# Kernel optimization log

Measured on AMD Instinct MI355X. Metric: run time of the kernel, lower is better.

## Reference

```python
import jax, jax.numpy as jnp
import numpy as np

N = 100000      # nodes
E = 1600000     # edges
F_IN = 256      # nfeat
F_OUT = 128     # out channels


def setup_inputs() -> dict:
    key = jax.random.key(0)
    k1, k2, k3 = jax.random.split(key, 3)
    feature = jax.random.normal(k1, (N, F_IN), dtype=jnp.float32)
    edge_index = jax.random.randint(k2, (2, E), 0, N, dtype=jnp.int32)
    # glorot-ish init for the GCN linear weight
    W = jax.random.normal(k3, (F_IN, F_OUT), dtype=jnp.float32) * (1.0 / np.sqrt(F_IN))
    b = jnp.zeros((F_OUT,), dtype=jnp.float32)
    return {"feature": feature, "edge_index": edge_index, "W": W, "b": b}


def reference(feature, edge_index, W, b):
    # GCNConv (PyG defaults): add self-loops, symmetric normalization,
    # linear transform then scatter-add aggregation to destination nodes.
    x = feature @ W                                   # [N, F_OUT]
    loops = jnp.arange(N, dtype=edge_index.dtype)
    row = jnp.concatenate([edge_index[0], loops])     # source nodes [E+N]
    col = jnp.concatenate([edge_index[1], loops])     # dest   nodes [E+N]
    ones = jnp.ones(row.shape[0], dtype=x.dtype)
    deg = jax.ops.segment_sum(ones, col, num_segments=N)   # in-degree incl. self-loop
    dinv = jnp.where(deg > 0, jax.lax.rsqrt(deg), 0.0)     # deg^{-1/2}
    norm = dinv[row] * dinv[col]                            # [E+N]
    msg = x[row] * norm[:, None]                            # gather + scale
    agg = jax.ops.segment_sum(msg, col, num_segments=N)     # scatter-add
    x_out = jax.nn.relu(agg + b)                            # [N, F_OUT]
    h = jax.nn.sigmoid(jnp.mean(x_out, axis=0))             # [F_OUT]
    return (x_out, h)
```

## Files before the change

kernel.cpp:

```cpp
#include <hip/hip_runtime.h>
#include <hip/hip_bf16.h>

typedef __attribute__((ext_vector_type(8))) short short8;
typedef __attribute__((ext_vector_type(4))) float floatx4;
typedef unsigned short u16;
typedef unsigned int u32;

#define F_IN  256
#define F_OUT 128
#define CAP   64
#define NWIN  8

__device__ __forceinline__ float bf_lo(u32 u) { return __uint_as_float(u << 16); }
__device__ __forceinline__ float bf_hi(u32 u) { return __uint_as_float(u & 0xffff0000u); }
__device__ __forceinline__ u16 f2bf(float f) {
    u32 u = __float_as_uint(f);
    u += 0x7fffu + ((u >> 16) & 1u);
    return (u16)(u >> 16);
}

__global__ void k_pack(const float* __restrict__ W, u16* __restrict__ Wp) {
    int gid = blockIdx.x * 256 + threadIdx.x;
    if (gid >= 32768) return;
    int f = gid >> 3, j = gid & 7;
    int lane = f & 63, tt = (f >> 6) & 7, kb = f >> 9;
    int m = lane & 15, q = lane >> 4;
    Wp[(size_t)f * 8 + j] = f2bf(W[(kb * 32 + q * 8 + j) * F_OUT + tt * 16 + m]);
}

__global__ void k_fillcap_xcd(const int* __restrict__ rowi, const int* __restrict__ coli,
                              int E, int npw, int N,
                              int* __restrict__ cursor, int* __restrict__ csr) {
    int grp  = blockIdx.x & (NWIN - 1);
    int gblk = blockIdx.x >> 3;
    int nblk = gridDim.x >> 3;
    int lo = grp * npw;
    int hi = lo + npw; if (hi > N) hi = N;
    for (int e = gblk * blockDim.x + threadIdx.x; e < E; e += nblk * blockDim.x) {
        int d = coli[e];
        if (d >= lo && d < hi) {
            int r = rowi[e];
            int p = atomicAdd(&cursor[d], 1);
            if (p < CAP) csr[((size_t)d << 6) + p] = r;
        }
    }
}

__global__ void k_degree(const int* __restrict__ col, int E, int* __restrict__ deg) {
    for (int e = blockIdx.x * blockDim.x + threadIdx.x; e < E; e += gridDim.x * blockDim.x)
        atomicAdd(&deg[col[e]], 1);
}

__global__ void k_blocksum(const int* __restrict__ deg, int N, int* __restrict__ bsum) {
    __shared__ int s[256];
    int base = blockIdx.x * 1024, t = threadIdx.x;
    int v = 0;
    for (int i = t; i < 1024; i += 256) { int idx = base + i; v += (idx < N) ? deg[idx] : 0; }
    s[t] = v; __syncthreads();
    for (int off = 128; off > 0; off >>= 1) {
        if (t < off) s[t] += s[t + off];
        __syncthreads();
    }
    if (t == 0) bsum[blockIdx.x] = s[0];
}

__global__ void k_rowptr(const int* __restrict__ deg, int N, const int* __restrict__ bsum,
                         int nb, int* __restrict__ rowptr) {
    __shared__ int s[256];
    __shared__ int sb[256];
    int base = blockIdx.x * 1024, t = threadIdx.x;
    sb[t] = (t < nb && t < blockIdx.x) ? bsum[t] : 0;
    __syncthreads();
    for (int off = 128; off > 0; off >>= 1) {
        if (t < off) sb[t] += sb[t + off];
        __syncthreads();
    }
    int blockbase = sb[0];
    int v[4]; int tot = 0;
#pragma unroll
    for (int j = 0; j < 4; ++j) {
        int idx = base + t * 4 + j;
        v[j] = (idx < N) ? deg[idx] : 0;
        tot += v[j];
    }
    s[t] = tot; __syncthreads();
    for (int off = 1; off < 256; off <<= 1) {
        int x = (t >= off) ? s[t - off] : 0;
        __syncthreads();
        s[t] += x;
        __syncthreads();
    }
    int prefix = blockbase + s[t] - tot;
#pragma unroll
    for (int j = 0; j < 4; ++j) {
        int idx = base + t * 4 + j;
        if (idx < N) rowptr[idx] = prefix;
        prefix += v[j];
    }
}

__global__ void k_fill(const int* __restrict__ rowi, const int* __restrict__ coli, int E,
                       const int* __restrict__ rowptr, int* __restrict__ cursor,
                       int* __restrict__ csr) {
    for (int e = blockIdx.x * blockDim.x + threadIdx.x; e < E; e += gridDim.x * blockDim.x) {
        int d = coli[e];
        int p = atomicAdd(&cursor[d], 1);
        csr[rowptr[d] + p] = rowi[e];
    }
}

__global__ __launch_bounds__(256) void k_gemm(
        const float* __restrict__ feat, const int* __restrict__ deg,
        const u16* __restrict__ Wp, u16* __restrict__ xw, int N) {
    __shared__ u16 atile[64 * 264];
    const int t = threadIdx.x, wave = t >> 6, lane = t & 63;
    const int m = lane & 15, q = lane >> 4;
    const int base = blockIdx.x * 64;

    for (int r = wave; r < 64; r += 4) {
        int i = base + r;
        float ax = 0.f, ay = 0.f, az = 0.f, aw = 0.f;
        if (i < N) {
            float di = rsqrtf((float)(deg[i] + 1));
            float4 v = *(const float4*)(feat + (size_t)i * F_IN + lane * 4);
            ax = di * v.x; ay = di * v.y; az = di * v.z; aw = di * v.w;
        }
        u32* dst = (u32*)(atile + r * 264 + lane * 4);
        dst[0] = ((u32)f2bf(ay) << 16) | (u32)f2bf(ax);
        dst[1] = ((u32)f2bf(aw) << 16) | (u32)f2bf(az);
    }
    __syncthreads();

    floatx4 acc[8];
#pragma unroll
    for (int tt = 0; tt < 8; ++tt) acc[tt] = (floatx4)0.0f;
    const short8* wp = (const short8*)Wp;
#pragma unroll
    for (int kb = 0; kb < 8; ++kb) {
        short8 a0 = *(const short8*)(atile + (wave * 16 + m) * 264 + kb * 32 + q * 8);
#pragma unroll
        for (int tt = 0; tt < 8; ++tt) {
            short8 b = wp[(kb * 8 + tt) * 64 + lane];
            acc[tt] = __builtin_amdgcn_mfma_f32_16x16x32_bf16(a0, b, acc[tt], 0, 0, 0);
        }
    }

#pragma unroll
    for (int r = 0; r < 4; ++r) {
        int orow = base + wave * 16 + q * 4 + r;
        if (orow < N) {
#pragma unroll
            for (int tt = 0; tt < 8; ++tt)
                xw[(size_t)orow * F_OUT + tt * 16 + m] = f2bf(acc[tt][r]);
        }
    }
}

__global__ __launch_bounds__(256) void k_agg(const u16* __restrict__ xw,
                                             const int* __restrict__ rowptr,
                                             const int* __restrict__ deg,
                                             const int* __restrict__ csr,
                                             const float* __restrict__ bvec,
                                             float* __restrict__ out,
                                             float* __restrict__ hsum, int N) {
    __shared__ float hpart[128];
    int t = threadIdx.x;
    if (t < 128) hpart[t] = 0.f;
    __syncthreads();
    int wave = t >> 6, lane = t & 63;
    const u32* xw32 = (const u32*)xw;
    float b0 = bvec[2 * lane], b1 = bvec[2 * lane + 1];
    float h0 = 0.f, h1 = 0.f;
    for (int i = blockIdx.x * 4 + wave; i < N; i += gridDim.x * 4) {
        int dd = deg[i];
        float di = rsqrtf((float)(dd + 1));
        int s0;
        if (rowptr) s0 = rowptr[i];
        else { s0 = i << 6; dd = dd < CAP ? dd : CAP; }
        u32 xs = xw32[(size_t)i * 64 + lane];
        float a0 = bf_lo(xs), a1 = bf_hi(xs);
        int j = 0;
        for (; j + 7 < dd; j += 8) {
            int sx[8]; u32 xv[8];
#pragma unroll
            for (int u = 0; u < 8; ++u) sx[u] = csr[s0 + j + u];
#pragma unroll
            for (int u = 0; u < 8; ++u) xv[u] = xw32[(size_t)sx[u] * 64 + lane];
#pragma unroll
            for (int u = 0; u < 8; ++u) { a0 += bf_lo(xv[u]); a1 += bf_hi(xv[u]); }
        }
        for (; j + 3 < dd; j += 4) {
            int sx[4]; u32 xv[4];
#pragma unroll
            for (int u = 0; u < 4; ++u) sx[u] = csr[s0 + j + u];
#pragma unroll
            for (int u = 0; u < 4; ++u) xv[u] = xw32[(size_t)sx[u] * 64 + lane];
#pragma unroll
            for (int u = 0; u < 4; ++u) { a0 += bf_lo(xv[u]); a1 += bf_hi(xv[u]); }
        }
        for (; j < dd; ++j) {
            u32 xA = xw32[(size_t)csr[s0 + j] * 64 + lane];
            a0 += bf_lo(xA);
            a1 += bf_hi(xA);
        }
        float o0 = fmaxf(fmaf(a0, di, b0), 0.f);
        float o1 = fmaxf(fmaf(a1, di, b1), 0.f);
        h0 += o0; h1 += o1;
        *(float2*)(out + (size_t)i * F_OUT + lane * 2) = make_float2(o0, o1);
    }
    atomicAdd(&hpart[2 * lane], h0);
    atomicAdd(&hpart[2 * lane + 1], h1);
    __syncthreads();
    if (t < 128) atomicAdd(&hsum[t], hpart[t]);
}

__global__ void k_h(const float* __restrict__ hsum, float* __restrict__ outh, float invN) {
    int t = threadIdx.x;
    if (t < 128) {
        float mm = hsum[t] * invN;
        outh[t] = 1.f / (1.f + __expf(-mm));
    }
}

extern "C" void kernel_launch(void* const* d_in, const int* in_sizes, int n_in,
                              void* d_out, int out_size, void* d_ws, size_t ws_size,
                              hipStream_t stream) {
    const float* feat = (const float*)d_in[0];
    const int* ei     = (const int*)d_in[1];
    const float* W    = (const float*)d_in[2];
    const float* bvec = (const float*)d_in[3];
    float* out        = (float*)d_out;

    const int N = in_sizes[0] / F_IN;
    const int E = in_sizes[1] / 2;

    char* ws = (char*)d_ws;
    size_t o = 0;
    u16* Wp       = (u16*)(ws + o);   o += (size_t)F_IN * F_OUT * 2;
    int* deg      = (int*)(ws + o);   o += (size_t)N * 4;
    int* cursor   = (int*)(ws + o);   o += (size_t)N * 4;
    float* hsum   = (float*)(ws + o); o += 512;
    int* rowptr   = (int*)(ws + o);   o += (size_t)N * 4;
    int* bsum     = (int*)(ws + o);   o += 1024;
    size_t fixed  = o;

    size_t need_fast = fixed + (size_t)N * CAP * 4 + (size_t)N * F_OUT * 2;
    bool fast = ws_size >= need_fast + 4096;

    if (fast) {
        int* csr = (int*)(ws + o);    o += (size_t)N * CAP * 4;
        u16* xw  = (u16*)(ws + o);    o += (size_t)N * F_OUT * 2;

        hipMemsetAsync((char*)cursor, 0, (size_t)N * 4 + 512, stream);
        k_pack<<<128, 256, 0, stream>>>(W, Wp);
        int npw = (N + NWIN - 1) / NWIN;
        k_fillcap_xcd<<<2048, 256, 0, stream>>>(ei, ei + E, E, npw, N, cursor, csr);
        int ntiles = (N + 63) / 64;
        k_gemm<<<ntiles, 256, 0, stream>>>(feat, cursor, Wp, xw, N);
        k_agg<<<2048, 256, 0, stream>>>(xw, nullptr, cursor, csr, bvec, out, hsum, N);
        k_h<<<1, 128, 0, stream>>>(hsum, out + (size_t)N * F_OUT, 1.0f / (float)N);
    } else {
        int* csr = (int*)(ws + o);    o += (size_t)E * 4;
        u16* xw  = (u16*)(ws + o);    o += (size_t)N * F_OUT * 2;

        hipMemsetAsync((char*)deg, 0, (size_t)N * 8 + 512, stream);
        k_pack<<<128, 256, 0, stream>>>(W, Wp);
        k_degree<<<1024, 256, 0, stream>>>(ei + E, E, deg);
        int nb = (N + 1023) / 1024;
        k_blocksum<<<nb, 256, 0, stream>>>(deg, N, bsum);
        k_rowptr<<<nb, 256, 0, stream>>>(deg, N, bsum, nb, rowptr);
        k_fill<<<1024, 256, 0, stream>>>(ei, ei + E, E, rowptr, cursor, csr);
        int ntiles = (N + 63) / 64;
        k_gemm<<<ntiles, 256, 0, stream>>>(feat, deg, Wp, xw, N);
        k_agg<<<2048, 256, 0, stream>>>(xw, rowptr, deg, csr, bvec, out, hsum, N);
        k_h<<<1, 128, 0, stream>>>(hsum, out + (size_t)N * F_OUT, 1.0f / (float)N);
    }
}
```

Baseline: 385.9 us.

## Slice xw into per-XCD column stripes and gather 8 nodes per wave

The GEMM now writes xw as 8 column slices of 16 features each, stored slice-major. The aggregation kernel assigns each block to one slice by blockIdx & 7, and each wave processes 8 nodes with 8 lanes per node, fetching neighbor indices cooperatively through shuffles. The intent is that each XCD only touches one ~3.2MB slice, so it can stay resident in that XCD's L2 instead of repeatedly missing to the infinity cache or HBM. In exchange, each gather is only 32B wide, and lanes within a wave wait for the node with the largest degree. Correctness also depends on the grid size being a multiple of 8.

New measurement: 372.1 us. -3.6%, faster.

```diff
diff --git a/kernel.cpp b/kernel.cpp
--- a/kernel.cpp
+++ b/kernel.cpp
@@ -151,7 +151,7 @@
         if (orow < N) {
 #pragma unroll
             for (int tt = 0; tt < 8; ++tt)
-                xw[(size_t)orow * F_OUT + tt * 16 + m] = f2bf(acc[tt][r]);
+                xw[((size_t)tt * N + orow) * 16 + m] = f2bf(acc[tt][r]);
         }
     }
 }
@@ -163,55 +163,58 @@
                                              const float* __restrict__ bvec,
                                              float* __restrict__ out,
                                              float* __restrict__ hsum, int N) {
-    __shared__ float hpart[128];
+    __shared__ float hpart[16];
     int t = threadIdx.x;
-    if (t < 128) hpart[t] = 0.f;
-    __syncthreads();
-    int wave = t >> 6, lane = t & 63;
-    const u32* xw32 = (const u32*)xw;
-    float b0 = bvec[2 * lane], b1 = bvec[2 * lane + 1];
+    if (t < 16) hpart[t] = 0.f;
+    __syncthreads();
+    const int w = blockIdx.x & 7;
+    const int stripe = blockIdx.x >> 3;
+    const int nstripe = gridDim.x >> 3;
+    const int lane = t & 63, wv = t >> 6;
+    const int lane7 = lane & 7;
+    const int g = lane >> 3;
+    const int gbase = lane & 56;
+    const u32* slice = (const u32*)xw + (size_t)w * N * 8;
+    float b0 = bvec[w * 16 + 2 * lane7], b1 = bvec[w * 16 + 2 * lane7 + 1];
     float h0 = 0.f, h1 = 0.f;
-    for (int i = blockIdx.x * 4 + wave; i < N; i += gridDim.x * 4) {
+    const int step = nstripe * 32;
+    for (int i = stripe * 32 + wv * 8 + g; i < N; i += step) {
         int dd = deg[i];
         float di = rsqrtf((float)(dd + 1));
         int s0;
         if (rowptr) s0 = rowptr[i];
         else { s0 = i << 6; dd = dd < CAP ? dd : CAP; }
-        u32 xs = xw32[(size_t)i * 64 + lane];
+        u32 xs = slice[(size_t)i * 8 + lane7];
         float a0 = bf_lo(xs), a1 = bf_hi(xs);
-        int j = 0;
-        for (; j + 7 < dd; j += 8) {
-            int sx[8]; u32 xv[8];
-#pragma unroll
-            for (int u = 0; u < 8; ++u) sx[u] = csr[s0 + j + u];
-#pragma unroll
-            for (int u = 0; u < 8; ++u) xv[u] = xw32[(size_t)sx[u] * 64 + lane];
-#pragma unroll
-            for (int u = 0; u < 8; ++u) { a0 += bf_lo(xv[u]); a1 += bf_hi(xv[u]); }
-        }
-        for (; j + 3 < dd; j += 4) {
-            int sx[4]; u32 xv[4];
-#pragma unroll
-            for (int u = 0; u < 4; ++u) sx[u] = csr[s0 + j + u];
-#pragma unroll
-            for (int u = 0; u < 4; ++u) xv[u] = xw32[(size_t)sx[u] * 64 + lane];
-#pragma unroll
-            for (int u = 0; u < 4; ++u) { a0 += bf_lo(xv[u]); a1 += bf_hi(xv[u]); }
-        }
-        for (; j < dd; ++j) {
-            u32 xA = xw32[(size_t)csr[s0 + j] * 64 + lane];
-            a0 += bf_lo(xA);
-            a1 += bf_hi(xA);
+        int ddmax = dd;
+        ddmax = max(ddmax, __shfl_xor(ddmax, 8));
+        ddmax = max(ddmax, __shfl_xor(ddmax, 16));
+        ddmax = max(ddmax, __shfl_xor(ddmax, 32));
+        for (int jb = 0; jb < ddmax; jb += 8) {
+            int sxv = 0;
+            if (jb + lane7 < dd) sxv = csr[s0 + jb + lane7];
+            u32 xv[8];
+#pragma unroll
+            for (int u = 0; u < 8; ++u) {
+                int sx = __shfl(sxv, gbase + u);
+                xv[u] = slice[(size_t)sx * 8 + lane7];
+            }
+#pragma unroll
+            for (int u = 0; u < 8; ++u) {
+                bool live = (jb + u < dd);
+                a0 += live ? bf_lo(xv[u]) : 0.f;
+                a1 += live ? bf_hi(xv[u]) : 0.f;
+            }
         }
         float o0 = fmaxf(fmaf(a0, di, b0), 0.f);
         float o1 = fmaxf(fmaf(a1, di, b1), 0.f);
         h0 += o0; h1 += o1;
-        *(float2*)(out + (size_t)i * F_OUT + lane * 2) = make_float2(o0, o1);
-    }
-    atomicAdd(&hpart[2 * lane], h0);
-    atomicAdd(&hpart[2 * lane + 1], h1);
-    __syncthreads();
-    if (t < 128) atomicAdd(&hsum[t], hpart[t]);
+        *(float2*)(out + (size_t)i * F_OUT + w * 16 + 2 * lane7) = make_float2(o0, o1);
+    }
+    atomicAdd(&hpart[2 * lane7], h0);
+    atomicAdd(&hpart[2 * lane7 + 1], h1);
+    __syncthreads();
+    if (t < 16) atomicAdd(&hsum[w * 16 + t], hpart[t]);
 }
 
 __global__ void k_h(const float* __restrict__ hsum, float* __restrict__ outh, float invN) {
```
